# Optimization experiments

Hardware: AMD Instinct MI355X
Metric: run time of the kernel (lower is better)

Reference implementation:

```python
import jax, jax.numpy as jnp
import numpy as np

N = 8_388_608
T_MAX = 4096


def setup_inputs() -> dict:
    key = jax.random.key(0)
    k1, k2, k3 = jax.random.split(key, 3)
    risk = jax.random.normal(k1, (N,), dtype=jnp.float32)
    time = jax.random.randint(k2, (N,), 0, T_MAX, dtype=jnp.int64)
    event = jax.random.randint(k3, (N,), 0, 2, dtype=jnp.int64)
    return {"risk": risk, "time": time, "event": event}


def reference(risk, time, event):
    # Sort descending by time (matches torch.argsort(time, descending=True)).
    order = jnp.argsort(-time)
    r = risk[order]            # [N] risk sorted by descending time
    t = time[order]            # [N]
    e = event[order] > 0       # [N] bool

    n = r.shape[0]
    # Cumulative (prefix) logsumexp over descending-sorted risks.
    # At-risk set for time t is exactly the prefix ending at the LAST index
    # of t's tie group, so log_denom(group) = clse[last_idx_of_group].
    clse = jax.lax.associative_scan(jnp.logaddexp, r)  # [N]

    # Last index of each contiguous tie block (times equal => contiguous after sort).
    is_last = jnp.concatenate([t[:-1] != t[1:], jnp.ones((1,), dtype=bool)])
    idx = jnp.arange(n)
    cand = jnp.where(is_last, idx, n)          # non-last positions -> sentinel
    last_idx = jax.lax.cummin(cand, axis=0, reverse=True)  # min over j >= i

    log_denom = clse[last_idx]                 # [N] per-sample group denominator

    # nll = -sum_groups(sum_{events in group} risk  -  d_group * log_denom)
    #     =  sum_{i: event_i} (log_denom_i - risk_i)
    nll = jnp.sum(jnp.where(e, log_denom - r, jnp.float32(0.0)))

    has_events = jnp.sum(event > 0) > 0
    return jnp.where(has_events, nll, jnp.float32(0.0))
```

## Files before the change

kernel.cpp:

```cpp
#include <hip/hip_runtime.h>
#include <hip/hip_fp16.h>

#define TMAX 4096
#define ABLOCKS 512
#define ATHREADS 1024
#define PERTHREAD_V4 4

#define SCALE_F 1048576.0f
#define INV_SCALE 9.5367431640625e-07f
#define SUM_MASK 0xFFFFFFFFFFFFULL
#define CNT_SHIFT 48

#define RB 64
#define RS 16
#define RBLOCKS (TMAX / RB)

__global__ __launch_bounds__(ATHREADS, 8) void coxph_hist_fixed(
    const float* __restrict__ risk, const int* __restrict__ time_,
    const int* __restrict__ event,
    unsigned* __restrict__ ppack, float* __restrict__ pevr,
    unsigned* __restrict__ done)
{
    __shared__ unsigned long long s_acc[TMAX];
    __shared__ float s_evr[ATHREADS / 64];

    const int tid = threadIdx.x;
    if (blockIdx.x == 0 && tid == 0) *done = 0u;
    #pragma unroll
    for (int k = 0; k < TMAX / ATHREADS; ++k) s_acc[tid + k * ATHREADS] = 0ull;
    __syncthreads();

    const float4* r4 = (const float4*)risk;
    const int4*   t4 = (const int4*)time_;
    const int4*   e4 = (const int4*)event;

    const int base = blockIdx.x * ATHREADS + tid;
    const int STRIDE4 = ABLOCKS * ATHREADS;

    float4 r[PERTHREAD_V4]; int4 t[PERTHREAD_V4]; int4 e[PERTHREAD_V4];
    #pragma unroll
    for (int k = 0; k < PERTHREAD_V4; ++k) {
        const int i = base + k * STRIDE4;
        r[k] = r4[i]; t[k] = t4[i]; e[k] = e4[i];
    }

    float evr = 0.f;
    #pragma unroll
    for (int k = 0; k < PERTHREAD_V4; ++k) {
        {
            unsigned lo = (unsigned)(__expf(r[k].x) * SCALE_F + 0.5f);
            unsigned long long pk = ((unsigned long long)(unsigned)e[k].x << CNT_SHIFT) | lo;
            atomicAdd(&s_acc[t[k].x & (TMAX - 1)], pk);
            evr += e[k].x ? r[k].x : 0.f;
        }
        {
            unsigned lo = (unsigned)(__expf(r[k].y) * SCALE_F + 0.5f);
            unsigned long long pk = ((unsigned long long)(unsigned)e[k].y << CNT_SHIFT) | lo;
            atomicAdd(&s_acc[t[k].y & (TMAX - 1)], pk);
            evr += e[k].y ? r[k].y : 0.f;
        }
        {
            unsigned lo = (unsigned)(__expf(r[k].z) * SCALE_F + 0.5f);
            unsigned long long pk = ((unsigned long long)(unsigned)e[k].z << CNT_SHIFT) | lo;
            atomicAdd(&s_acc[t[k].z & (TMAX - 1)], pk);
            evr += e[k].z ? r[k].z : 0.f;
        }
        {
            unsigned lo = (unsigned)(__expf(r[k].w) * SCALE_F + 0.5f);
            unsigned long long pk = ((unsigned long long)(unsigned)e[k].w << CNT_SHIFT) | lo;
            atomicAdd(&s_acc[t[k].w & (TMAX - 1)], pk);
            evr += e[k].w ? r[k].w : 0.f;
        }
    }

    #pragma unroll
    for (int off = 32; off > 0; off >>= 1) evr += __shfl_down(evr, off);
    const int lane = tid & 63, wave = tid >> 6;
    if (lane == 0) s_evr[wave] = evr;
    __syncthreads();

    unsigned* pp = ppack + (size_t)blockIdx.x * TMAX;
    #pragma unroll
    for (int k = 0; k < TMAX / ATHREADS; ++k) {
        const int i = tid + k * ATHREADS;
        unsigned long long v = s_acc[i];
        float s = (float)(v & SUM_MASK) * INV_SCALE;
        unsigned c = (unsigned)(v >> CNT_SHIFT);
        unsigned hb = (unsigned)__half_as_ushort(__float2half(s));
        pp[i] = (c << 16) | hb;
    }
    if (tid == 0) {
        float tot = 0.f;
        for (int w = 0; w < ATHREADS / 64; ++w) tot += s_evr[w];
        pevr[blockIdx.x] = tot;
    }
}

__global__ __launch_bounds__(ATHREADS, 8) void coxph_hist_generic(
    const float* __restrict__ risk, const int* __restrict__ time_,
    const int* __restrict__ event,
    unsigned* __restrict__ ppack, float* __restrict__ pevr,
    unsigned* __restrict__ done, int n)
{
    __shared__ unsigned long long s_acc[TMAX];
    __shared__ float s_evr[ATHREADS / 64];

    const int tid = threadIdx.x;
    if (blockIdx.x == 0 && tid == 0) *done = 0u;
    #pragma unroll
    for (int k = 0; k < TMAX / ATHREADS; ++k) s_acc[tid + k * ATHREADS] = 0ull;
    __syncthreads();

    float evr = 0.f;
    const int stride = gridDim.x * ATHREADS;
    for (int i = blockIdx.x * ATHREADS + tid; i < n; i += stride) {
        float rv = risk[i];
        int   ev = event[i];
        unsigned lo = (unsigned)(__expf(rv) * SCALE_F + 0.5f);
        unsigned long long pk = ((unsigned long long)(unsigned)ev << CNT_SHIFT) | lo;
        atomicAdd(&s_acc[time_[i] & (TMAX - 1)], pk);
        evr += ev ? rv : 0.f;
    }

    #pragma unroll
    for (int off = 32; off > 0; off >>= 1) evr += __shfl_down(evr, off);
    const int lane = tid & 63, wave = tid >> 6;
    if (lane == 0) s_evr[wave] = evr;
    __syncthreads();

    unsigned* pp = ppack + (size_t)blockIdx.x * TMAX;
    #pragma unroll
    for (int k = 0; k < TMAX / ATHREADS; ++k) {
        const int i = tid + k * ATHREADS;
        unsigned long long v = s_acc[i];
        float s = (float)(v & SUM_MASK) * INV_SCALE;
        unsigned c = (unsigned)(v >> CNT_SHIFT);
        unsigned hb = (unsigned)__half_as_ushort(__float2half(s));
        pp[i] = (c << 16) | hb;
    }
    if (tid == 0) {
        float tot = 0.f;
        for (int w = 0; w < ATHREADS / 64; ++w) tot += s_evr[w];
        pevr[blockIdx.x] = tot;
    }
}

__global__ __launch_bounds__(1024) void coxph_reduce_finalize(
    const unsigned* __restrict__ ppack, const float* __restrict__ pevr,
    float* __restrict__ bsum, unsigned* __restrict__ bcnt,
    unsigned* __restrict__ done, float* __restrict__ out)
{
    __shared__ float    ls[RS * RB];
    __shared__ unsigned lc[RS * RB];
    __shared__ unsigned s_last;

    const int t = threadIdx.x;
    const int j = t & (RB - 1);
    const int s = t >> 6;
    const int bucket = blockIdx.x * RB + j;

    float sum = 0.f; unsigned cnt = 0u;
    #pragma unroll
    for (int k = 0; k < ABLOCKS / RS; ++k) {
        const int row = s * (ABLOCKS / RS) + k;
        unsigned p = ppack[(size_t)row * TMAX + bucket];
        sum += __half2float(__ushort_as_half((unsigned short)(p & 0xFFFFu)));
        cnt += p >> 16;
    }
    ls[t] = sum; lc[t] = cnt;
    __syncthreads();

    #pragma unroll
    for (int h = RS / 2; h >= 1; h >>= 1) {
        if (s < h) { ls[t] += ls[t + h * RB]; lc[t] += lc[t + h * RB]; }
        __syncthreads();
    }
    if (s == 0) { bsum[bucket] = ls[j]; bcnt[bucket] = lc[j]; }
    __syncthreads();

    if (t == 0) {
        __threadfence();
        unsigned old = atomicAdd(done, 1u);
        s_last = (old == RBLOCKS - 1) ? 1u : 0u;
    }
    __syncthreads();
    if (!s_last) return;
    __threadfence();

    __shared__ float    s_wsum[16];
    __shared__ double   s_dacc[16];
    __shared__ unsigned s_cacc[16];

    const int lane = t & 63, wave = t >> 6;
    const int j0 = 4 * t;
    float v0 = bsum[TMAX - 1 - j0];
    float v1 = bsum[TMAX - 2 - j0];
    float v2 = bsum[TMAX - 3 - j0];
    float v3 = bsum[TMAX - 4 - j0];
    float p0 = v0, p1 = p0 + v1, p2 = p1 + v2, p3 = p2 + v3;

    float t_incl = p3;
    #pragma unroll
    for (int off = 1; off < 64; off <<= 1) {
        float u = __shfl_up(t_incl, off);
        if (lane >= off) t_incl += u;
    }
    if (lane == 63) s_wsum[wave] = t_incl;
    __syncthreads();
    if (t == 0) {
        float acc = 0.f;
        for (int w = 0; w < 16; ++w) { float x = s_wsum[w]; s_wsum[w] = acc; acc += x; }
    }
    __syncthreads();
    const float excl = (t_incl - p3) + s_wsum[wave];

    double acc = 0.0;
    unsigned ctot = 0u;
    unsigned c0 = bcnt[TMAX - 1 - j0];
    unsigned c1 = bcnt[TMAX - 2 - j0];
    unsigned c2 = bcnt[TMAX - 3 - j0];
    unsigned c3 = bcnt[TMAX - 4 - j0];
    if (c0) { acc += (double)c0 * (double)logf(excl + p0); ctot += c0; }
    if (c1) { acc += (double)c1 * (double)logf(excl + p1); ctot += c1; }
    if (c2) { acc += (double)c2 * (double)logf(excl + p2); ctot += c2; }
    if (c3) { acc += (double)c3 * (double)logf(excl + p3); ctot += c3; }

    if (t < ABLOCKS) acc -= (double)pevr[t];

    #pragma unroll
    for (int off = 32; off > 0; off >>= 1) {
        acc  += __shfl_down(acc, off);
        ctot += __shfl_down(ctot, off);
    }
    if (lane == 0) { s_dacc[wave] = acc; s_cacc[wave] = ctot; }
    __syncthreads();
    if (t == 0) {
        double a = 0.0; unsigned c = 0u;
        for (int w = 0; w < 16; ++w) { a += s_dacc[w]; c += s_cacc[w]; }
        out[0] = c ? (float)a : 0.0f;
    }
}

extern "C" void kernel_launch(void* const* d_in, const int* in_sizes, int n_in,
                              void* d_out, int out_size, void* d_ws, size_t ws_size,
                              hipStream_t stream)
{
    const float* risk  = (const float*)d_in[0];
    const int*   time_ = (const int*)d_in[1];
    const int*   event = (const int*)d_in[2];
    float* out = (float*)d_out;
    const int n = in_sizes[0];

    char* ws = (char*)d_ws;
    size_t off = 0;
    unsigned* ppack = (unsigned*)(ws + off); off += (size_t)ABLOCKS * TMAX * sizeof(unsigned);
    float*    pevr  = (float*)(ws + off);    off += ABLOCKS * sizeof(float);
    float*    bsum  = (float*)(ws + off);    off += TMAX * sizeof(float);
    unsigned* bcnt  = (unsigned*)(ws + off); off += TMAX * sizeof(unsigned);
    unsigned* done  = (unsigned*)(ws + off); off += sizeof(unsigned);

    if (n == ABLOCKS * ATHREADS * 4 * PERTHREAD_V4) {
        coxph_hist_fixed<<<ABLOCKS, ATHREADS, 0, stream>>>(
            risk, time_, event, ppack, pevr, done);
    } else {
        coxph_hist_generic<<<ABLOCKS, ATHREADS, 0, stream>>>(
            risk, time_, event, ppack, pevr, done, n);
    }
    coxph_reduce_finalize<<<RBLOCKS, RS * RB, 0, stream>>>(
        ppack, pevr, bsum, bcnt, done, out);
}
```

Measured before the change: 127.0 us.

## Split shared histogram into two wave-group copies and emit per-wave event sums

The fixed-size histogram kernel now keeps two shared-memory histogram copies. Each half of the block's waves does its atomics into its own copy, so LDS atomic contention is halved, and the two copies are summed when results are written out. Per-wave event-risk sums now go straight to global memory instead of through a shared reduction done by thread 0, and the finalize kernel sums them. This doubles LDS use to 64KB per block, which may lower occupancy, and adds a larger global buffer of partial sums.

```diff
diff --git a/kernel.cpp b/kernel.cpp
--- a/kernel.cpp
+++ b/kernel.cpp
@@ -4,6 +4,7 @@
 #define TMAX 4096
 #define ABLOCKS 512
 #define ATHREADS 1024
+#define NWAVES (ATHREADS / 64)
 #define PERTHREAD_V4 4
 
 #define SCALE_F 1048576.0f
@@ -18,17 +19,19 @@
 __global__ __launch_bounds__(ATHREADS, 8) void coxph_hist_fixed(
     const float* __restrict__ risk, const int* __restrict__ time_,
     const int* __restrict__ event,
-    unsigned* __restrict__ ppack, float* __restrict__ pevr,
+    unsigned* __restrict__ ppack, float* __restrict__ pevr_waves,
     unsigned* __restrict__ done)
 {
-    __shared__ unsigned long long s_acc[TMAX];
-    __shared__ float s_evr[ATHREADS / 64];
+    __shared__ unsigned long long s_acc[2 * TMAX];
 
     const int tid = threadIdx.x;
     if (blockIdx.x == 0 && tid == 0) *done = 0u;
     #pragma unroll
-    for (int k = 0; k < TMAX / ATHREADS; ++k) s_acc[tid + k * ATHREADS] = 0ull;
-    __syncthreads();
+    for (int k = 0; k < 2 * TMAX / ATHREADS; ++k) s_acc[tid + k * ATHREADS] = 0ull;
+    __syncthreads();
+
+    const int lane = tid & 63, wave = tid >> 6;
+    unsigned long long* __restrict__ hist = s_acc + ((wave >= NWAVES / 2) ? TMAX : 0);
 
     const float4* r4 = (const float4*)risk;
     const int4*   t4 = (const int4*)time_;
@@ -50,60 +53,53 @@
         {
             unsigned lo = (unsigned)(__expf(r[k].x) * SCALE_F + 0.5f);
             unsigned long long pk = ((unsigned long long)(unsigned)e[k].x << CNT_SHIFT) | lo;
-            atomicAdd(&s_acc[t[k].x & (TMAX - 1)], pk);
+            atomicAdd(&hist[t[k].x & (TMAX - 1)], pk);
             evr += e[k].x ? r[k].x : 0.f;
         }
         {
             unsigned lo = (unsigned)(__expf(r[k].y) * SCALE_F + 0.5f);
             unsigned long long pk = ((unsigned long long)(unsigned)e[k].y << CNT_SHIFT) | lo;
-            atomicAdd(&s_acc[t[k].y & (TMAX - 1)], pk);
+            atomicAdd(&hist[t[k].y & (TMAX - 1)], pk);
             evr += e[k].y ? r[k].y : 0.f;
         }
         {
             unsigned lo = (unsigned)(__expf(r[k].z) * SCALE_F + 0.5f);
             unsigned long long pk = ((unsigned long long)(unsigned)e[k].z << CNT_SHIFT) | lo;
-            atomicAdd(&s_acc[t[k].z & (TMAX - 1)], pk);
+            atomicAdd(&hist[t[k].z & (TMAX - 1)], pk);
             evr += e[k].z ? r[k].z : 0.f;
         }
         {
             unsigned lo = (unsigned)(__expf(r[k].w) * SCALE_F + 0.5f);
             unsigned long long pk = ((unsigned long long)(unsigned)e[k].w << CNT_SHIFT) | lo;
-            atomicAdd(&s_acc[t[k].w & (TMAX - 1)], pk);
+            atomicAdd(&hist[t[k].w & (TMAX - 1)], pk);
             evr += e[k].w ? r[k].w : 0.f;
         }
     }
 
     #pragma unroll
     for (int off = 32; off > 0; off >>= 1) evr += __shfl_down(evr, off);
-    const int lane = tid & 63, wave = tid >> 6;
-    if (lane == 0) s_evr[wave] = evr;
+    if (lane == 0) pevr_waves[blockIdx.x * NWAVES + wave] = evr;
     __syncthreads();
 
     unsigned* pp = ppack + (size_t)blockIdx.x * TMAX;
     #pragma unroll
     for (int k = 0; k < TMAX / ATHREADS; ++k) {
         const int i = tid + k * ATHREADS;
-        unsigned long long v = s_acc[i];
+        unsigned long long v = s_acc[i] + s_acc[i + TMAX];
         float s = (float)(v & SUM_MASK) * INV_SCALE;
         unsigned c = (unsigned)(v >> CNT_SHIFT);
         unsigned hb = (unsigned)__half_as_ushort(__float2half(s));
         pp[i] = (c << 16) | hb;
     }
-    if (tid == 0) {
-        float tot = 0.f;
-        for (int w = 0; w < ATHREADS / 64; ++w) tot += s_evr[w];
-        pevr[blockIdx.x] = tot;
-    }
 }
 
 __global__ __launch_bounds__(ATHREADS, 8) void coxph_hist_generic(
     const float* __restrict__ risk, const int* __restrict__ time_,
     const int* __restrict__ event,
-    unsigned* __restrict__ ppack, float* __restrict__ pevr,
+    unsigned* __restrict__ ppack, float* __restrict__ pevr_waves,
     unsigned* __restrict__ done, int n)
 {
     __shared__ unsigned long long s_acc[TMAX];
-    __shared__ float s_evr[ATHREADS / 64];
 
     const int tid = threadIdx.x;
     if (blockIdx.x == 0 && tid == 0) *done = 0u;
@@ -125,7 +121,7 @@
     #pragma unroll
     for (int off = 32; off > 0; off >>= 1) evr += __shfl_down(evr, off);
     const int lane = tid & 63, wave = tid >> 6;
-    if (lane == 0) s_evr[wave] = evr;
+    if (lane == 0) pevr_waves[blockIdx.x * NWAVES + wave] = evr;
     __syncthreads();
 
     unsigned* pp = ppack + (size_t)blockIdx.x * TMAX;
@@ -138,15 +134,10 @@
         unsigned hb = (unsigned)__half_as_ushort(__float2half(s));
         pp[i] = (c << 16) | hb;
     }
-    if (tid == 0) {
-        float tot = 0.f;
-        for (int w = 0; w < ATHREADS / 64; ++w) tot += s_evr[w];
-        pevr[blockIdx.x] = tot;
-    }
 }
 
 __global__ __launch_bounds__(1024) void coxph_reduce_finalize(
-    const unsigned* __restrict__ ppack, const float* __restrict__ pevr,
+    const unsigned* __restrict__ ppack, const float* __restrict__ pevr_waves,
     float* __restrict__ bsum, unsigned* __restrict__ bcnt,
     unsigned* __restrict__ done, float* __restrict__ out)
 {
@@ -225,7 +216,13 @@
     if (c2) { acc += (double)c2 * (double)logf(excl + p2); ctot += c2; }
     if (c3) { acc += (double)c3 * (double)logf(excl + p3); ctot += c3; }
 
-    if (t < ABLOCKS) acc -= (double)pevr[t];
+    {
+        float ev = 0.f;
+        #pragma unroll
+        for (int k = 0; k < (ABLOCKS * NWAVES) / 1024; ++k)
+            ev += pevr_waves[t * ((ABLOCKS * NWAVES) / 1024) + k];
+        acc -= (double)ev;
+    }
 
     #pragma unroll
     for (int off = 32; off > 0; off >>= 1) {
@@ -254,7 +251,7 @@
     char* ws = (char*)d_ws;
     size_t off = 0;
     unsigned* ppack = (unsigned*)(ws + off); off += (size_t)ABLOCKS * TMAX * sizeof(unsigned);
-    float*    pevr  = (float*)(ws + off);    off += ABLOCKS * sizeof(float);
+    float*    pevr  = (float*)(ws + off);    off += (size_t)ABLOCKS * NWAVES * sizeof(float);
     float*    bsum  = (float*)(ws + off);    off += TMAX * sizeof(float);
     unsigned* bcnt  = (unsigned*)(ws + off); off += TMAX * sizeof(unsigned);
     unsigned* done  = (unsigned*)(ws + off); off += sizeof(unsigned);
```

After: 129.0 us. Within noise of the previous version (+1.6%).
